# Optimization experiments

Measured on AMD Instinct MI355X. Metric: run time of the kernel, lower is better.

The kernel has to match this reference:

```python
import jax, jax.numpy as jnp
import numpy as np

B, T, D = 2, 2048, 1024
NH, NKV, HD = 16, 4, 64
KD = NKV * HD          # 256
PD = 16                # rope partial dim (rotated dims)
RANK = 8
ALPHA = 1.0
ROPE_BASE = 10000.0


def setup_inputs() -> dict:
    key = jax.random.key(0)
    ks = jax.random.split(key, 10)
    s = 0.02
    return {
        "x":      jax.random.normal(ks[0], (B, T, D), jnp.float32),
        "Wq":     jax.random.normal(ks[1], (D, D), jnp.float32) * s,
        "Wk":     jax.random.normal(ks[2], (KD, D), jnp.float32) * s,
        "Wv":     jax.random.normal(ks[3], (KD, D), jnp.float32) * s,
        "Wproj":  jax.random.normal(ks[4], (D, D), jnp.float32) * s,
        "q_gain": jnp.full((NH,), 5.25, jnp.float32),
        "Aq":     jax.random.normal(ks[5], (RANK, D), jnp.float32) * s,
        "Bq":     jax.random.normal(ks[6], (D, RANK), jnp.float32) * s,
        "Av":     jax.random.normal(ks[7], (RANK, D), jnp.float32) * s,
        "Bv":     jax.random.normal(ks[8], (KD, RANK), jnp.float32) * s,
    }


def _rms_norm(x):
    # F.rms_norm with no weight: x / sqrt(mean(x^2) + eps), eps = dtype machine eps
    eps = jnp.finfo(x.dtype).eps
    return x * jax.lax.rsqrt(jnp.mean(x * x, axis=-1, keepdims=True) + eps)


def _rope_partial(x, cos, sin, pd):
    # x: [B, T, H, HD]; rotate first pd dims (half/half), pass rest through
    h = pd // 2
    x1, x2, rest = x[..., :h], x[..., h:pd], x[..., pd:]
    c = cos[None, :, None, :]  # [1, T, 1, h]
    s = sin[None, :, None, :]
    return jnp.concatenate([x1 * c + x2 * s, -x2 * c + x1 * s, rest], axis=-1)


def reference(x, Wq, Wk, Wv, Wproj, q_gain, Aq, Bq, Av, Bv):
    # projections + per-step LoRA on Q and V (output = alpha * B(A(x)))
    q = x @ Wq.T + ALPHA * ((x @ Aq.T) @ Bq.T)          # [B,T,D]
    k = x @ Wk.T                                        # [B,T,KD]
    v = x @ Wv.T + ALPHA * ((x @ Av.T) @ Bv.T)          # [B,T,KD]

    q = _rms_norm(q.reshape(B, T, NH, HD))
    k = _rms_norm(k.reshape(B, T, NKV, HD))
    v = v.reshape(B, T, NKV, HD)

    # partial RoPE tables: [T, PD//2]
    inv = 1.0 / (ROPE_BASE ** (jnp.arange(0, PD, 2, dtype=jnp.float32) / PD))
    freqs = jnp.arange(T, dtype=jnp.float32)[:, None] * inv[None, :]
    cos, sin = jnp.cos(freqs), jnp.sin(freqs)
    q = _rope_partial(q, cos, sin, PD)
    k = _rope_partial(k, cos, sin, PD)

    # learned per-head QK gain on queries
    q = q * q_gain[None, None, :, None]

    # GQA: repeat-interleave kv heads to NH
    g = NH // NKV
    kf = jnp.repeat(k, g, axis=2)  # [B,T,NH,HD]
    vf = jnp.repeat(v, g, axis=2)

    scale = 1.0 / np.float32(np.sqrt(HD))
    scores = jnp.einsum('bqhd,bkhd->bhqk', q, kf) * scale  # [B,NH,T,T]
    causal = jnp.tril(jnp.ones((T, T), bool))
    scores = jnp.where(causal[None, None], scores, -jnp.inf)
    p = jax.nn.softmax(scores, axis=-1)
    y = jnp.einsum('bhqk,bkhd->bqhd', p, vf).reshape(B, T, D)
    return y @ Wproj.T
```

## Files before the change

kernel.cpp:

```cpp
#include <hip/hip_runtime.h>

#define Tn   2048
#define Dn   1024
#define KDn  256
#define NHn  16
#define NKVn 4
#define Rn   4096

typedef short bf16x8 __attribute__((ext_vector_type(8)));
typedef float f32x4  __attribute__((ext_vector_type(4)));
typedef const __attribute__((address_space(1))) unsigned* gas_p;
typedef __attribute__((address_space(3))) unsigned* las_p;

__device__ unsigned short g_q[(size_t)Rn * Dn];
__device__ unsigned short g_k[(size_t)Rn * KDn];
__device__ unsigned short g_vt[(size_t)2 * NKVn * 64 * Tn];
__device__ unsigned short g_y[(size_t)Rn * Dn];
__device__ unsigned short g_xb[(size_t)Rn * Dn];
__device__ unsigned short g_wq[(size_t)Dn * Dn];
__device__ unsigned short g_wk[(size_t)KDn * Dn];
__device__ unsigned short g_wv[(size_t)KDn * Dn];
__device__ unsigned short g_wp[(size_t)Dn * Dn];
__device__ float g_tq[Rn * 8];
__device__ float g_tv[Rn * 8];

static __device__ __forceinline__ float bf2f(unsigned short u) {
    return __uint_as_float(((unsigned)u) << 16);
}
static __device__ __forceinline__ unsigned short f2bf(float f) {
    unsigned u = __float_as_uint(f);
    u += 0x7fffu + ((u >> 16) & 1u);
    return (unsigned short)(u >> 16);
}
static __device__ __forceinline__ unsigned pk2bf(float a, float b) {
    return (unsigned)f2bf(a) | ((unsigned)f2bf(b) << 16);
}
static __device__ __forceinline__ unsigned cvtpk(float a, float b) {
    unsigned r;
    asm("v_cvt_pk_bf16_f32 %0, %1, %2" : "=v"(r) : "v"(a), "v"(b));
    return r;
}
static __device__ __forceinline__ float wave_sum(float s) {
    #pragma unroll
    for (int off = 32; off; off >>= 1) s += __shfl_xor(s, off);
    return s;
}

#define NQ4 (Dn * Dn / 4)
#define NK4 (KDn * Dn / 4)
#define CASTB ((NQ4 * 2 + NK4 * 2) / 256)
__global__ __launch_bounds__(256)
void prep(const float* __restrict__ x,
          const float* __restrict__ Aq,
          const float* __restrict__ Av,
          const float* __restrict__ Wq, const float* __restrict__ Wk,
          const float* __restrict__ Wv, const float* __restrict__ Wp) {
    if (blockIdx.x < CASTB) {
        int i = blockIdx.x * 256 + threadIdx.x;
        const float* src; unsigned short* dst; int o;
        if      (i < NQ4)                 { src = Wq; dst = g_wq; o = i; }
        else if (i < NQ4 + NK4)           { src = Wk; dst = g_wk; o = i - NQ4; }
        else if (i < NQ4 + 2 * NK4)       { src = Wv; dst = g_wv; o = i - NQ4 - NK4; }
        else                              { src = Wp; dst = g_wp; o = i - NQ4 - 2 * NK4; }
        float4 v = ((const float4*)src)[o];
        ((uint2*)dst)[o] = make_uint2(pk2bf(v.x, v.y), pk2bf(v.z, v.w));
        return;
    }
    int tid = threadIdx.x, wave = tid >> 6, lane = tid & 63;
    int row = (blockIdx.x - CASTB) * 4 + wave;
    const float4* xr = (const float4*)(x + (size_t)row * Dn);
    uint2* xbo = (uint2*)g_xb + (size_t)row * (Dn / 4);
    float aq[8], av[8];
    #pragma unroll
    for (int r = 0; r < 8; r++) { aq[r] = 0.f; av[r] = 0.f; }
    for (int it = 0; it < Dn / 256; it++) {
        int j = it * 64 + lane;
        float4 xv = xr[j];
        xbo[j] = make_uint2(pk2bf(xv.x, xv.y), pk2bf(xv.z, xv.w));
        #pragma unroll
        for (int r = 0; r < 8; r++) {
            float4 a4 = ((const float4*)(Aq + (size_t)r * Dn))[j];
            aq[r] += xv.x * a4.x + xv.y * a4.y + xv.z * a4.z + xv.w * a4.w;
        }
        #pragma unroll
        for (int r = 0; r < 8; r++) {
            float4 a4 = ((const float4*)(Av + (size_t)r * Dn))[j];
            av[r] += xv.x * a4.x + xv.y * a4.y + xv.z * a4.z + xv.w * a4.w;
        }
    }
    #pragma unroll
    for (int r = 0; r < 8; r++) { aq[r] = wave_sum(aq[r]); av[r] = wave_sum(av[r]); }
    if (lane == 0) {
        #pragma unroll
        for (int r = 0; r < 8; r++) { g_tq[row * 8 + r] = aq[r]; g_tv[row * 8 + r] = av[r]; }
    }
}

template<int MODE>
__global__ __launch_bounds__(256, 2)
void gemm_bt(float* __restrict__ Cout, const float* __restrict__ BqL,
             const float* __restrict__ BvL, const float* __restrict__ qgain,
             int M, int K) {
    const unsigned short* A = (MODE == 0) ? g_xb : g_y;

    int gx = gridDim.x;
    int flat = blockIdx.y * gx + blockIdx.x;
    int cpx = (gx * gridDim.y) >> 3;
    int flat2 = (flat & 7) * cpx + (flat >> 3);
    int n0 = (flat2 % gx) * 64, m0 = (flat2 / gx) * 128;

    const unsigned short* W;
    int wroff, region;
    if (MODE == 0) {
        if (n0 < 1024)      { W = g_wq; wroff = n0;        region = 0; }
        else if (n0 < 1280) { W = g_wk; wroff = n0 - 1024; region = 1; }
        else                { W = g_wv; wroff = n0 - 1280; region = 2; }
    } else { W = g_wp; wroff = n0; region = 3; }

    __shared__ __align__(16) unsigned short SM[24576];
    int tid = threadIdx.x;
    int w = tid >> 6, lane = tid & 63;
    int m_ = lane & 15, quad = lane >> 4;

    int lrow = lane >> 3, lseg = (lane & 7) * 8;
    const unsigned short* agp[4];
    #pragma unroll
    for (int i = 0; i < 4; i++)
        agp[i] = A + (size_t)(m0 + w * 32 + i * 8 + lrow) * K + lseg;
    const unsigned short* wgp[2];
    #pragma unroll
    for (int i = 0; i < 2; i++)
        wgp[i] = W + (size_t)(wroff + w * 16 + i * 8 + lrow) * K + lseg;
    int alb[4], wlb[2];
    #pragma unroll
    for (int i = 0; i < 4; i++) alb[i] = (w * 32 + i * 8) * 64;
    #pragma unroll
    for (int i = 0; i < 2; i++) wlb[i] = 16384 + (w * 16 + i * 8) * 64;

    f32x4 acc[2][4];
    #pragma unroll
    for (int im = 0; im < 2; im++)
        #pragma unroll
        for (int in = 0; in < 4; in++) acc[im][in] = (f32x4){0.f, 0.f, 0.f, 0.f};

    #pragma unroll
    for (int i = 0; i < 4; i++)
        __builtin_amdgcn_global_load_lds((gas_p)agp[i], (las_p)&SM[alb[i]], 16, 0, 0);
    #pragma unroll
    for (int i = 0; i < 2; i++)
        __builtin_amdgcn_global_load_lds((gas_p)wgp[i], (las_p)&SM[wlb[i]], 16, 0, 0);

    int nk = K >> 6;
    for (int kt = 0; kt < nk; kt++) {
        __syncthreads();
        int cur = kt & 1, nxt = cur ^ 1;
        if (kt + 1 < nk) {
            int ko = (kt + 1) * 64;
            #pragma unroll
            for (int i = 0; i < 4; i++)
                __builtin_amdgcn_global_load_lds((gas_p)(agp[i] + ko),
                    (las_p)&SM[nxt * 8192 + alb[i]], 16, 0, 0);
            #pragma unroll
            for (int i = 0; i < 2; i++)
                __builtin_amdgcn_global_load_lds((gas_p)(wgp[i] + ko),
                    (las_p)&SM[wlb[i] + nxt * 4096], 16, 0, 0);
        }
        #pragma unroll
        for (int kk = 0; kk < 2; kk++) {
            bf16x8 bf[4];
            #pragma unroll
            for (int in = 0; in < 4; in++)
                bf[in] = *(const bf16x8*)&SM[16384 + cur * 4096 +
                                             (in * 16 + m_) * 64 + kk * 32 + quad * 8];
            #pragma unroll
            for (int im = 0; im < 2; im++) {
                bf16x8 af = *(const bf16x8*)&SM[cur * 8192 +
                                                (w * 32 + im * 16 + m_) * 64 + kk * 32 + quad * 8];
                #pragma unroll
                for (int in = 0; in < 4; in++)
                    acc[im][in] = __builtin_amdgcn_mfma_f32_16x16x32_bf16(af, bf[in], acc[im][in], 0, 0, 0);
            }
        }
    }

    if (MODE == 1) {
        #pragma unroll
        for (int im = 0; im < 2; im++)
            #pragma unroll
            for (int r = 0; r < 4; r++) {
                int row = m0 + w * 32 + im * 16 + quad * 4 + r;
                #pragma unroll
                for (int in = 0; in < 4; in++)
                    Cout[(size_t)row * Dn + (n0 + in * 16 + m_)] = acc[im][in][r];
            }
        return;
    }

    if (region <= 1) {
        float blc[4][8];
        if (region == 0) {
            #pragma unroll
            for (int in = 0; in < 4; in++) {
                const float* bp = BqL + (size_t)(n0 + in * 16 + m_) * 8;
                #pragma unroll
                for (int j = 0; j < 8; j++) blc[in][j] = bp[j];
            }
        }
        float ghead = (region == 0) ? qgain[n0 >> 6] * 0.18033688011112042f : 1.0f;
        #pragma unroll
        for (int im = 0; im < 2; im++) {
            #pragma unroll
            for (int r = 0; r < 4; r++) {
                int row = m0 + w * 32 + im * 16 + quad * 4 + r;
                float vv[4];
                float ss = 0.f;
                if (region == 0) {
                    const float* tp = g_tq + (size_t)row * 8;
                    float tv8[8];
                    #pragma unroll
                    for (int j = 0; j < 8; j++) tv8[j] = tp[j];
                    #pragma unroll
                    for (int in = 0; in < 4; in++) {
                        float val = acc[im][in][r];
                        #pragma unroll
                        for (int j = 0; j < 8; j++) val += tv8[j] * blc[in][j];
                        vv[in] = val; ss += val * val;
                    }
                } else {
                    #pragma unroll
                    for (int in = 0; in < 4; in++) { vv[in] = acc[im][in][r]; ss += vv[in] * vv[in]; }
                }
                ss += __shfl_xor(ss, 1); ss += __shfl_xor(ss, 2);
                ss += __shfl_xor(ss, 4); ss += __shfl_xor(ss, 8);
                float rs = rsqrtf(ss * (1.0f / 64.0f) + 1.1920929e-7f);
                #pragma unroll
                for (int in = 0; in < 4; in++) vv[in] *= rs;
                float p = __shfl_xor(vv[0], 8);
                int t = row & (Tn - 1);
                float fr = (float)t * exp2f(-(float)(m_ & 7) * 1.6609640474436813f);
                float c = cosf(fr), sn = sinf(fr);
                if (m_ < 16) vv[0] = (m_ < 8) ? vv[0] * c + p * sn : p * sn - vv[0] * c;
                #pragma unroll
                for (int in = 0; in < 4; in++) {
                    float val = vv[in] * ghead;
                    int col = n0 + in * 16 + m_;
                    if (region == 0) g_q[(size_t)row * Dn + col] = f2bf(val);
                    else             g_k[(size_t)row * KDn + (col - 1024)] = f2bf(val);
                }
            }
        }
    } else {
        float blc[4][8];
        #pragma unroll
        for (int in = 0; in < 4; in++) {
            const float* bp = BvL + (size_t)(n0 - 1280 + in * 16 + m_) * 8;
            #pragma unroll
            for (int j = 0; j < 8; j++) blc[in][j] = bp[j];
        }
        __syncthreads();
        #pragma unroll
        for (int im = 0; im < 2; im++) {
            #pragma unroll
            for (int r = 0; r < 4; r++) {
                int rl = w * 32 + im * 16 + quad * 4 + r;
                const float* tp = g_tv + (size_t)(m0 + rl) * 8;
                float tv8[8];
                #pragma unroll
                for (int j = 0; j < 8; j++) tv8[j] = tp[j];
                #pragma unroll
                for (int in = 0; in < 4; in++) {
                    float val = acc[im][in][r];
                    #pragma unroll
                    for (int j = 0; j < 8; j++) val += tv8[j] * blc[in][j];
                    SM[(in * 16 + m_) * 136 + rl] = f2bf(val);
                }
            }
        }
        __syncthreads();
        int d = tid >> 2, tseg = (tid & 3) * 32;
        int bb = m0 >> 11, t0 = m0 & (Tn - 1);
        int kvh = (n0 - 1280) >> 6;
        unsigned short* dst = g_vt + (((size_t)(bb * NKVn + kvh) * 64) + d) * Tn + t0 + tseg;
        const uint4* srcv = (const uint4*)&SM[d * 136 + tseg];
        uint4 c0 = srcv[0], c1 = srcv[1], c2 = srcv[2], c3 = srcv[3];
        ((uint4*)dst)[0] = c0; ((uint4*)dst)[1] = c1;
        ((uint4*)dst)[2] = c2; ((uint4*)dst)[3] = c3;
    }
}

__global__ __launch_bounds__(256, 4)
void attn_kernel() {
    __shared__ __align__(16) unsigned short KS[64 * 72];
    __shared__ __align__(16) unsigned short VS[64 * 72];
    __shared__ __align__(16) unsigned short Pt[4][16 * 72];
    int tid = threadIdx.x;
    int w = tid >> 6, lane = tid & 63;
    int q_ = lane & 15, quad = lane >> 4;
    int b = blockIdx.z, kvh = blockIdx.y, h = kvh * 4 + w;
    int bx = blockIdx.x;
    if ((kvh >> 1) & 1) bx = 127 - bx;
    int qb = bx * 16;
    int qg = qb + q_;

    const unsigned short* qrow =
        g_q + ((size_t)(b * Tn + qg) * NHn + h) * 64 + quad * 8;
    bf16x8 Qf0 = *(const bf16x8*)qrow;
    bf16x8 Qf1 = *(const bf16x8*)(qrow + 32);

    int srow = tid >> 2, sseg = (tid & 3) * 16;
    const unsigned short* kgp =
        g_k + ((size_t)(b * Tn + srow) * NKVn + kvh) * 64 + sseg;
    const unsigned short* vgp =
        g_vt + ((size_t)(b * NKVn + kvh) * 64 + srow) * Tn + sseg;

    f32x4 accO[4];
    #pragma unroll
    for (int i = 0; i < 4; i++) accO[i] = (f32x4){0.f, 0.f, 0.f, 0.f};
    float lsum = 0.f;
    int ntiles = (qb + 79) >> 6;

    {
        uint4 ka = *(const uint4*)kgp, kb = *(const uint4*)(kgp + 8);
        uint4 va = *(const uint4*)vgp, vb = *(const uint4*)(vgp + 8);
        *(uint4*)&KS[srow * 72 + sseg] = ka;
        *(uint4*)&KS[srow * 72 + sseg + 8] = kb;
        *(uint4*)&VS[srow * 72 + sseg] = va;
        *(uint4*)&VS[srow * 72 + sseg + 8] = vb;
    }
    __syncthreads();

    for (int kt = 0; kt < ntiles; kt++) {
        bool pre = (kt + 1 < ntiles);
        uint4 kan, kbn, van, vbn;
        if (pre) {
            const unsigned short* kp = kgp + (size_t)(kt + 1) * (64 * NKVn * 64);
            const unsigned short* vp = vgp + (kt + 1) * 64;
            kan = *(const uint4*)kp; kbn = *(const uint4*)(kp + 8);
            van = *(const uint4*)vp; vbn = *(const uint4*)(vp + 8);
        }

        f32x4 s[4];
        __builtin_amdgcn_s_setprio(1);
        #pragma unroll
        for (int ss = 0; ss < 4; ss++) {
            bf16x8 ka = *(const bf16x8*)&KS[(ss * 16 + q_) * 72 + quad * 8];
            bf16x8 kb = *(const bf16x8*)&KS[(ss * 16 + q_) * 72 + 32 + quad * 8];
            s[ss] = (f32x4){0.f, 0.f, 0.f, 0.f};
            s[ss] = __builtin_amdgcn_mfma_f32_16x16x32_bf16(ka, Qf0, s[ss], 0, 0, 0);
            s[ss] = __builtin_amdgcn_mfma_f32_16x16x32_bf16(kb, Qf1, s[ss], 0, 0, 0);
        }
        __builtin_amdgcn_s_setprio(0);

        if (kt == ntiles - 1) {
            #pragma unroll
            for (int ss = 0; ss < 4; ss++) {
                int k0 = kt * 64 + ss * 16 + quad * 4;
                #pragma unroll
                for (int r = 0; r < 4; r++)
                    if (k0 + r > qg) s[ss][r] = -1e30f;
            }
        }
        float p[4][4];
        #pragma unroll
        for (int ss = 0; ss < 4; ss++)
            #pragma unroll
            for (int r = 0; r < 4; r++) {
                p[ss][r] = exp2f(s[ss][r]);
                lsum += p[ss][r];
            }

        unsigned short* pb = &Pt[w][0];
        #pragma unroll
        for (int ss = 0; ss < 4; ss++)
            *(uint2*)&pb[q_ * 72 + ss * 16 + quad * 4] =
                make_uint2(cvtpk(p[ss][0], p[ss][1]), cvtpk(p[ss][2], p[ss][3]));
        bf16x8 pf0 = *(const bf16x8*)&pb[q_ * 72 + quad * 8];
        bf16x8 pf1 = *(const bf16x8*)&pb[q_ * 72 + 32 + quad * 8];

        __builtin_amdgcn_s_setprio(1);
        #pragma unroll
        for (int c = 0; c < 4; c++) {
            bf16x8 vf0 = *(const bf16x8*)&VS[(c * 16 + q_) * 72 + quad * 8];
            bf16x8 vf1 = *(const bf16x8*)&VS[(c * 16 + q_) * 72 + 32 + quad * 8];
            accO[c] = __builtin_amdgcn_mfma_f32_16x16x32_bf16(vf0, pf0, accO[c], 0, 0, 0);
            accO[c] = __builtin_amdgcn_mfma_f32_16x16x32_bf16(vf1, pf1, accO[c], 0, 0, 0);
        }
        __builtin_amdgcn_s_setprio(0);

        __syncthreads();
        if (pre) {
            *(uint4*)&KS[srow * 72 + sseg] = kan;
            *(uint4*)&KS[srow * 72 + sseg + 8] = kbn;
            *(uint4*)&VS[srow * 72 + sseg] = van;
            *(uint4*)&VS[srow * 72 + sseg + 8] = vbn;
        }
        __syncthreads();
    }

    lsum += __shfl_xor(lsum, 16);
    lsum += __shfl_xor(lsum, 32);
    float invl = 1.0f / lsum;
    unsigned short* yp = g_y + ((size_t)(b * Tn + qg) * NHn + h) * 64;
    #pragma unroll
    for (int c = 0; c < 4; c++) {
        uint2 o = make_uint2(cvtpk(accO[c][0] * invl, accO[c][1] * invl),
                             cvtpk(accO[c][2] * invl, accO[c][3] * invl));
        *(uint2*)&yp[c * 16 + quad * 4] = o;
    }
}

extern "C" void kernel_launch(void* const* d_in, const int* in_sizes, int n_in,
                              void* d_out, int out_size, void* d_ws, size_t ws_size,
                              hipStream_t stream) {
    const float* x  = (const float*)d_in[0];
    const float* Wq = (const float*)d_in[1];
    const float* Wk = (const float*)d_in[2];
    const float* Wv = (const float*)d_in[3];
    const float* Wp = (const float*)d_in[4];
    const float* qg = (const float*)d_in[5];
    const float* Aq = (const float*)d_in[6];
    const float* Bq = (const float*)d_in[7];
    const float* Av = (const float*)d_in[8];
    const float* Bv = (const float*)d_in[9];
    float* out = (float*)d_out;

    prep<<<dim3(CASTB + Rn / 4), dim3(256), 0, stream>>>(x, Aq, Av, Wq, Wk, Wv, Wp);
    gemm_bt<0><<<dim3(1536 / 64, Rn / 128), dim3(256), 0, stream>>>(
        nullptr, Bq, Bv, qg, Rn, Dn);
    attn_kernel<<<dim3(Tn / 16, NKVn, 2), dim3(256), 0, stream>>>();
    gemm_bt<1><<<dim3(Dn / 64, Rn / 128), dim3(256), 0, stream>>>(
        out, nullptr, nullptr, nullptr, Rn, Dn);
}
```

Measured before the change: 187.1 us.

## Enlarge projection GEMM tiles to 128x128 with 2x2 wave layout

Doubles the GEMM block tile along N so each wave computes a 64x64 sub-tile, increasing operand reuse from LDS and halving global loads of A per output. The epilogues (RMSNorm/RoPE for Q/K, V transpose) are adapted to handle two heads per block. This reduces block count to roughly one wave of blocks per CU and adds an extra barrier per k-step, which may reduce latency hiding.

```diff
diff --git a/kernel.cpp b/kernel.cpp
--- a/kernel.cpp
+++ b/kernel.cpp
@@ -107,7 +107,7 @@
     int flat = blockIdx.y * gx + blockIdx.x;
     int cpx = (gx * gridDim.y) >> 3;
     int flat2 = (flat & 7) * cpx + (flat >> 3);
-    int n0 = (flat2 % gx) * 64, m0 = (flat2 / gx) * 128;
+    int n0 = (flat2 % gx) * 128, m0 = (flat2 / gx) * 128;
 
     const unsigned short* W;
     int wroff, region;
@@ -117,9 +117,10 @@
         else                { W = g_wv; wroff = n0 - 1280; region = 2; }
     } else { W = g_wp; wroff = n0; region = 3; }
 
-    __shared__ __align__(16) unsigned short SM[24576];
+    __shared__ __align__(16) unsigned short SM[32768];
     int tid = threadIdx.x;
     int w = tid >> 6, lane = tid & 63;
+    int wr = w >> 1, wc = w & 1;
     int m_ = lane & 15, quad = lane >> 4;
 
     int lrow = lane >> 3, lseg = (lane & 7) * 8;
@@ -127,19 +128,19 @@
     #pragma unroll
     for (int i = 0; i < 4; i++)
         agp[i] = A + (size_t)(m0 + w * 32 + i * 8 + lrow) * K + lseg;
-    const unsigned short* wgp[2];
-    #pragma unroll
-    for (int i = 0; i < 2; i++)
-        wgp[i] = W + (size_t)(wroff + w * 16 + i * 8 + lrow) * K + lseg;
-    int alb[4], wlb[2];
+    const unsigned short* wgp[4];
+    #pragma unroll
+    for (int i = 0; i < 4; i++)
+        wgp[i] = W + (size_t)(wroff + w * 32 + i * 8 + lrow) * K + lseg;
+    int alb[4], wlb[4];
     #pragma unroll
     for (int i = 0; i < 4; i++) alb[i] = (w * 32 + i * 8) * 64;
     #pragma unroll
-    for (int i = 0; i < 2; i++) wlb[i] = 16384 + (w * 16 + i * 8) * 64;
-
-    f32x4 acc[2][4];
-    #pragma unroll
-    for (int im = 0; im < 2; im++)
+    for (int i = 0; i < 4; i++) wlb[i] = 16384 + (w * 32 + i * 8) * 64;
+
+    f32x4 acc[4][4];
+    #pragma unroll
+    for (int im = 0; im < 4; im++)
         #pragma unroll
         for (int in = 0; in < 4; in++) acc[im][in] = (f32x4){0.f, 0.f, 0.f, 0.f};
 
@@ -147,7 +148,7 @@
     for (int i = 0; i < 4; i++)
         __builtin_amdgcn_global_load_lds((gas_p)agp[i], (las_p)&SM[alb[i]], 16, 0, 0);
     #pragma unroll
-    for (int i = 0; i < 2; i++)
+    for (int i = 0; i < 4; i++)
         __builtin_amdgcn_global_load_lds((gas_p)wgp[i], (las_p)&SM[wlb[i]], 16, 0, 0);
 
     int nk = K >> 6;
@@ -161,37 +162,40 @@
                 __builtin_amdgcn_global_load_lds((gas_p)(agp[i] + ko),
                     (las_p)&SM[nxt * 8192 + alb[i]], 16, 0, 0);
             #pragma unroll
-            for (int i = 0; i < 2; i++)
+            for (int i = 0; i < 4; i++)
                 __builtin_amdgcn_global_load_lds((gas_p)(wgp[i] + ko),
-                    (las_p)&SM[wlb[i] + nxt * 4096], 16, 0, 0);
-        }
+                    (las_p)&SM[wlb[i] + nxt * 8192], 16, 0, 0);
+        }
+        __syncthreads();
         #pragma unroll
         for (int kk = 0; kk < 2; kk++) {
-            bf16x8 bf[4];
+            bf16x8 bfr[4];
             #pragma unroll
             for (int in = 0; in < 4; in++)
-                bf[in] = *(const bf16x8*)&SM[16384 + cur * 4096 +
-                                             (in * 16 + m_) * 64 + kk * 32 + quad * 8];
-            #pragma unroll
-            for (int im = 0; im < 2; im++) {
+                bfr[in] = *(const bf16x8*)&SM[16384 + cur * 8192 +
+                                              (wc * 64 + in * 16 + m_) * 64 + kk * 32 + quad * 8];
+            #pragma unroll
+            for (int im = 0; im < 4; im++) {
                 bf16x8 af = *(const bf16x8*)&SM[cur * 8192 +
-                                                (w * 32 + im * 16 + m_) * 64 + kk * 32 + quad * 8];
+                                                (wr * 64 + im * 16 + m_) * 64 + kk * 32 + quad * 8];
                 #pragma unroll
                 for (int in = 0; in < 4; in++)
-                    acc[im][in] = __builtin_amdgcn_mfma_f32_16x16x32_bf16(af, bf[in], acc[im][in], 0, 0, 0);
-            }
-        }
-    }
+                    acc[im][in] = __builtin_amdgcn_mfma_f32_16x16x32_bf16(af, bfr[in], acc[im][in], 0, 0, 0);
+            }
+        }
+    }
+
+    int colbase = n0 + wc * 64;
 
     if (MODE == 1) {
         #pragma unroll
-        for (int im = 0; im < 2; im++)
+        for (int im = 0; im < 4; im++)
             #pragma unroll
             for (int r = 0; r < 4; r++) {
-                int row = m0 + w * 32 + im * 16 + quad * 4 + r;
+                int row = m0 + wr * 64 + im * 16 + quad * 4 + r;
                 #pragma unroll
                 for (int in = 0; in < 4; in++)
-                    Cout[(size_t)row * Dn + (n0 + in * 16 + m_)] = acc[im][in][r];
+                    Cout[(size_t)row * Dn + (colbase + in * 16 + m_)] = acc[im][in][r];
             }
         return;
     }
@@ -201,17 +205,17 @@
         if (region == 0) {
             #pragma unroll
             for (int in = 0; in < 4; in++) {
-                const float* bp = BqL + (size_t)(n0 + in * 16 + m_) * 8;
+                const float* bp = BqL + (size_t)(colbase + in * 16 + m_) * 8;
                 #pragma unroll
                 for (int j = 0; j < 8; j++) blc[in][j] = bp[j];
             }
         }
-        float ghead = (region == 0) ? qgain[n0 >> 6] * 0.18033688011112042f : 1.0f;
-        #pragma unroll
-        for (int im = 0; im < 2; im++) {
+        float ghead = (region == 0) ? qgain[colbase >> 6] * 0.18033688011112042f : 1.0f;
+        #pragma unroll
+        for (int im = 0; im < 4; im++) {
             #pragma unroll
             for (int r = 0; r < 4; r++) {
-                int row = m0 + w * 32 + im * 16 + quad * 4 + r;
+                int row = m0 + wr * 64 + im * 16 + quad * 4 + r;
                 float vv[4];
                 float ss = 0.f;
                 if (region == 0) {
@@ -239,11 +243,11 @@
                 int t = row & (Tn - 1);
                 float fr = (float)t * exp2f(-(float)(m_ & 7) * 1.6609640474436813f);
                 float c = cosf(fr), sn = sinf(fr);
-                if (m_ < 16) vv[0] = (m_ < 8) ? vv[0] * c + p * sn : p * sn - vv[0] * c;
+                vv[0] = (m_ < 8) ? vv[0] * c + p * sn : p * sn - vv[0] * c;
                 #pragma unroll
                 for (int in = 0; in < 4; in++) {
                     float val = vv[in] * ghead;
-                    int col = n0 + in * 16 + m_;
+                    int col = colbase + in * 16 + m_;
                     if (region == 0) g_q[(size_t)row * Dn + col] = f2bf(val);
                     else             g_k[(size_t)row * KDn + (col - 1024)] = f2bf(val);
                 }
@@ -253,16 +257,16 @@
         float blc[4][8];
         #pragma unroll
         for (int in = 0; in < 4; in++) {
-            const float* bp = BvL + (size_t)(n0 - 1280 + in * 16 + m_) * 8;
+            const float* bp = BvL + (size_t)(colbase - 1280 + in * 16 + m_) * 8;
             #pragma unroll
             for (int j = 0; j < 8; j++) blc[in][j] = bp[j];
         }
         __syncthreads();
         #pragma unroll
-        for (int im = 0; im < 2; im++) {
+        for (int im = 0; im < 4; im++) {
             #pragma unroll
             for (int r = 0; r < 4; r++) {
-                int rl = w * 32 + im * 16 + quad * 4 + r;
+                int rl = wr * 64 + im * 16 + quad * 4 + r;
                 const float* tp = g_tv + (size_t)(m0 + rl) * 8;
                 float tv8[8];
                 #pragma unroll
@@ -272,19 +276,24 @@
                     float val = acc[im][in][r];
                     #pragma unroll
                     for (int j = 0; j < 8; j++) val += tv8[j] * blc[in][j];
-                    SM[(in * 16 + m_) * 136 + rl] = f2bf(val);
+                    int lc = wc * 64 + in * 16 + m_;
+                    SM[lc * 136 + rl] = f2bf(val);
                 }
             }
         }
         __syncthreads();
+        int bb = m0 >> 11, t0 = m0 & (Tn - 1);
+        int kvh0 = (n0 - 1280) >> 6;
         int d = tid >> 2, tseg = (tid & 3) * 32;
-        int bb = m0 >> 11, t0 = m0 & (Tn - 1);
-        int kvh = (n0 - 1280) >> 6;
-        unsigned short* dst = g_vt + (((size_t)(bb * NKVn + kvh) * 64) + d) * Tn + t0 + tseg;
-        const uint4* srcv = (const uint4*)&SM[d * 136 + tseg];
-        uint4 c0 = srcv[0], c1 = srcv[1], c2 = srcv[2], c3 = srcv[3];
-        ((uint4*)dst)[0] = c0; ((uint4*)dst)[1] = c1;
-        ((uint4*)dst)[2] = c2; ((uint4*)dst)[3] = c3;
+        #pragma unroll
+        for (int half = 0; half < 2; half++) {
+            unsigned short* dst = g_vt +
+                (((size_t)(bb * NKVn + kvh0 + half) * 64) + d) * Tn + t0 + tseg;
+            const uint4* srcv = (const uint4*)&SM[(half * 64 + d) * 136 + tseg];
+            uint4 c0 = srcv[0], c1 = srcv[1], c2 = srcv[2], c3 = srcv[3];
+            ((uint4*)dst)[0] = c0; ((uint4*)dst)[1] = c1;
+            ((uint4*)dst)[2] = c2; ((uint4*)dst)[3] = c3;
+        }
     }
 }
 
@@ -425,9 +434,9 @@
     float* out = (float*)d_out;
 
     prep<<<dim3(CASTB + Rn / 4), dim3(256), 0, stream>>>(x, Aq, Av, Wq, Wk, Wv, Wp);
-    gemm_bt<0><<<dim3(1536 / 64, Rn / 128), dim3(256), 0, stream>>>(
+    gemm_bt<0><<<dim3(1536 / 128, Rn / 128), dim3(256), 0, stream>>>(
         nullptr, Bq, Bv, qg, Rn, Dn);
     attn_kernel<<<dim3(Tn / 16, NKVn, 2), dim3(256), 0, stream>>>();
-    gemm_bt<1><<<dim3(Dn / 64, Rn / 128), dim3(256), 0, stream>>>(
+    gemm_bt<1><<<dim3(Dn / 128, Rn / 128), dim3(256), 0, stream>>>(
         out, nullptr, nullptr, nullptr, Rn, Dn);
 }
```

Result: slower. 212.5 us (+13.6%).
